# Kernel optimization log

Measured on AMD Instinct MI355X. Metric: run time of the kernel, lower is better.

The kernel has to match this reference:

```python
import jax, jax.numpy as jnp
import numpy as np

N = 102400          # total nodes (256 graphs x 400 nodes)
E = 3276800         # edges (avg degree 32)
B = 256             # num graphs
NODE_DIM, MRI_DIM, COG_DIM, CLIN_DIM, GEN_DIM, NUM_CLASSES = 128, 256, 64, 32, 512, 3
EPS = 1e-5

def _lin(k, i, o):
    kw, kb = jax.random.split(k)
    s = 1.0 / np.sqrt(i)
    return (jax.random.uniform(kw, (i, o), jnp.float32, -s, s),
            jax.random.uniform(kb, (o,), jnp.float32, -s, s))

def setup_inputs() -> dict:
    key = jax.random.key(0)
    ks = jax.random.split(key, 20)
    inp = {}
    inp['x'] = jax.random.normal(ks[0], (N, NODE_DIM), jnp.float32)
    inp['edge_index'] = jax.random.randint(ks[1], (2, E), 0, N)
    inp['batch'] = jnp.repeat(jnp.arange(B, dtype=jnp.int32), N // B)
    inp['mri'] = jax.random.normal(ks[2], (B, MRI_DIM), jnp.float32)
    inp['cog'] = jax.random.normal(ks[3], (B, COG_DIM), jnp.float32)
    inp['clin'] = jax.random.normal(ks[4], (B, CLIN_DIM), jnp.float32)
    inp['gen'] = jax.random.normal(ks[5], (B, GEN_DIM), jnp.float32)
    inp['W1'], inp['b1'] = _lin(ks[6], NODE_DIM, 64)
    inp['W2'], inp['b2'] = _lin(ks[7], 64, 32)
    inp['W3'], inp['b3'] = _lin(ks[8], 32, 16)
    inp['bn1_g'] = jnp.ones((64,), jnp.float32); inp['bn1_b'] = jnp.zeros((64,), jnp.float32)
    inp['bn2_g'] = jnp.ones((32,), jnp.float32); inp['bn2_b'] = jnp.zeros((32,), jnp.float32)
    inp['mriW'], inp['mrib'] = _lin(ks[9], MRI_DIM, 16)
    inp['cogW'], inp['cogb'] = _lin(ks[10], COG_DIM, 16)
    inp['clinW'], inp['clinb'] = _lin(ks[11], CLIN_DIM, 16)
    inp['genW'], inp['genb'] = _lin(ks[12], GEN_DIM, 16)
    inp['c1W'], inp['c1b'] = _lin(ks[13], 96, 64)  # 32 (pooled) + 64 (multimodal)
    inp['cbn1_g'] = jnp.ones((64,), jnp.float32); inp['cbn1_b'] = jnp.zeros((64,), jnp.float32)
    inp['c2W'], inp['c2b'] = _lin(ks[14], 64, 32)
    inp['cbn2_g'] = jnp.ones((32,), jnp.float32); inp['cbn2_b'] = jnp.zeros((32,), jnp.float32)
    inp['c3W'], inp['c3b'] = _lin(ks[15], 32, NUM_CLASSES)
    return inp

def _bn(h, g, b):
    # BatchNorm1d in training mode: biased batch stats
    m = h.mean(0)
    v = jnp.mean((h - m) ** 2, 0)
    return (h - m) * jax.lax.rsqrt(v + EPS) * g + b

def _gcn(h, W, bias, s, d, norm):
    # GCNConv: linear -> symmetric-normalized scatter-add aggregation (self-loops in s/d)
    h = h @ W
    agg = jnp.zeros_like(h).at[d].add(h[s] * norm[:, None])
    return agg + bias

def reference(x, edge_index, batch, mri, cog, clin, gen,
              W1, b1, W2, b2, W3, b3, bn1_g, bn1_b, bn2_g, bn2_b,
              mriW, mrib, cogW, cogb, clinW, clinb, genW, genb,
              c1W, c1b, cbn1_g, cbn1_b, c2W, c2b, cbn2_g, cbn2_b, c3W, c3b):
    n = x.shape[0]
    loop = jnp.arange(n)
    s = jnp.concatenate([edge_index[0], loop])
    d = jnp.concatenate([edge_index[1], loop])
    deg = jnp.zeros((n,), x.dtype).at[d].add(1.0)
    dinv = jax.lax.rsqrt(deg)  # deg >= 1 due to self-loops
    norm = dinv[s] * dinv[d]

    x1 = jax.nn.relu(_bn(_gcn(x, W1, b1, s, d, norm), bn1_g, bn1_b))
    x2 = jax.nn.relu(_bn(_gcn(x1, W2, b2, s, d, norm), bn2_g, bn2_b))
    gf = jax.nn.relu(_gcn(x2, W3, b3, s, d, norm))  # [N,16]

    cnt = jax.ops.segment_sum(jnp.ones((n,), x.dtype), batch, num_segments=B)
    g_mean = jax.ops.segment_sum(gf, batch, num_segments=B) / cnt[:, None]
    g_max = jax.ops.segment_max(gf, batch, num_segments=B)
    g_emb = jnp.concatenate([g_mean, g_max], axis=1)  # [B,32]

    mm = jnp.concatenate([
        jax.nn.relu(mri @ mriW + mrib),
        jax.nn.relu(cog @ cogW + cogb),
        jax.nn.relu(clin @ clinW + clinb),
        jax.nn.relu(gen @ genW + genb)], axis=1)  # [B,64]

    h = jnp.concatenate([g_emb, mm], axis=1)  # [B,96]
    h = jax.nn.relu(_bn(h @ c1W + c1b, cbn1_g, cbn1_b))  # dropout = identity (eval)
    h = jax.nn.relu(_bn(h @ c2W + c2b, cbn2_g, cbn2_b))
    out = h @ c3W + c3b
    return jax.nn.log_softmax(out, axis=1)
```

## Files before the change

### kernel.cpp

```cpp
#include <hip/hip_runtime.h>
#include <hip/hip_bf16.h>

#define TPB 256
#define BSHIFT 9
#define BNODES 512
#define CH 4096

typedef unsigned long long u64;
typedef __attribute__((ext_vector_type(8))) short short8;
typedef __attribute__((ext_vector_type(4))) float f32x4;

__device__ inline unsigned short f2bf(float f) {
    unsigned u = __float_as_uint(f);
    return (unsigned short)((u + 0x7FFF + ((u >> 16) & 1)) >> 16);
}
__device__ inline float bf2f(short s) {
    return __uint_as_float(((unsigned)(unsigned short)s) << 16);
}

__global__ void k_early(const float* __restrict__ x, unsigned short* __restrict__ xb, int npA,
                        const int* __restrict__ dstp, int* __restrict__ bcnt, int E,
                        int nbuk, int npart,
                        const float* __restrict__ W1, const float* __restrict__ W2,
                        const float* __restrict__ W3, unsigned short* __restrict__ Wpack) {
    __shared__ int h[256];
    int blk = blockIdx.x, tid = threadIdx.x;
    if (blk < npA) {
        int g = blk * TPB + tid;
        int lane = g & 63, tile = g >> 6;
        int rowblk = tile >> 2, kblk = tile & 3;
        int row = rowblk * 16 + (lane & 15);
        int k0 = kblk * 32 + (lane >> 4) * 8;
        const float4* p = reinterpret_cast<const float4*>(x + (size_t)row * 128 + k0);
        float4 v0 = p[0], v1 = p[1];
        float vs[8] = {v0.x, v0.y, v0.z, v0.w, v1.x, v1.y, v1.z, v1.w};
        short8 rr;
        #pragma unroll
        for (int u = 0; u < 8; ++u) rr[u] = (short)f2bf(vs[u]);
        *reinterpret_cast<short8*>(xb + (size_t)g * 8) = rr;
    } else if (blk < npA + npart) {
        int pb = blk - npA;
        h[tid] = 0;
        __syncthreads();
        int e0 = pb * CH;
        int e1 = min(e0 + CH, E);
        for (int e = e0 + tid; e < e1; e += TPB) atomicAdd(&h[dstp[e] >> BSHIFT], 1);
        __syncthreads();
        if (tid < nbuk && h[tid]) atomicAdd(&bcnt[tid], h[tid]);
    } else if (tid < 64) {
        int b = blk - npA - npart;
        const float* W; int KB, C; size_t off; int idx;
        if (b < 16)      { W = W1; KB = 4; C = 64; off = 0;     idx = b; }
        else if (b < 20) { W = W2; KB = 2; C = 32; off = 8192;  idx = b - 16; }
        else             { W = W3; KB = 1; C = 16; off = 10240; idx = b - 20; }
        int nblk = idx / KB, kblk = idx - nblk * KB;
        int col = nblk * 16 + (tid & 15);
        int k0 = kblk * 32 + (tid >> 4) * 8;
        short8 rr;
        #pragma unroll
        for (int j = 0; j < 8; ++j) rr[j] = (short)f2bf(W[(size_t)(k0 + j) * C + col]);
        *reinterpret_cast<short8*>(Wpack + off + ((size_t)idx * 64 + tid) * 8) = rr;
    }
}


__global__ void k_bscan(const int* __restrict__ bcnt, int* __restrict__ bbase,
                        int* __restrict__ gcur, int nbuk, int E) {
    __shared__ int s[256];
    int tid = threadIdx.x;
    int v = (tid < nbuk) ? bcnt[tid] : 0;
    s[tid] = v;
    __syncthreads();
    for (int o = 1; o < 256; o <<= 1) {
        int t = (tid >= o) ? s[tid - o] : 0;
        __syncthreads();
        s[tid] += t;
        __syncthreads();
    }
    if (tid < nbuk) { int e = s[tid] - v; bbase[tid] = e; gcur[tid] = e; }
    if (tid == 0) bbase[nbuk] = E;
}

__global__ void k_partition(const int* __restrict__ ei, int* __restrict__ gcur,
                            u64* __restrict__ part, int E, int nbuk) {
    __shared__ int h[256], baseg[256], scn[256], cur[256];
    __shared__ u64 stage[CH];
    int tid = threadIdx.x;
    h[tid] = 0;
    __syncthreads();
    int e0 = blockIdx.x * CH;
    int ecnt = min(CH, E - e0);
    const int* srcp = ei;
    const int* dstp = ei + E;
    for (int i = tid; i < ecnt; i += TPB) atomicAdd(&h[dstp[e0 + i] >> BSHIFT], 1);
    __syncthreads();
    int v = h[tid];
    if (tid < nbuk && v) baseg[tid] = atomicAdd(&gcur[tid], v);
    scn[tid] = v;
    __syncthreads();
    for (int o = 1; o < 256; o <<= 1) {
        int t = (tid >= o) ? scn[tid - o] : 0;
        __syncthreads();
        scn[tid] += t;
        __syncthreads();
    }
    int excl = scn[tid] - v;
    __syncthreads();
    scn[tid] = excl; cur[tid] = excl;
    __syncthreads();
    for (int i = tid; i < ecnt; i += TPB) {
        int s = srcp[e0 + i], d = dstp[e0 + i];
        int bk = d >> BSHIFT;
        int p = atomicAdd(&cur[bk], 1);
        stage[p] = ((u64)(unsigned)d << 32) | (unsigned)s;
    }
    __syncthreads();
    for (int i = tid; i < ecnt; i += TPB) {
        u64 vv = stage[i];
        int bk = (int)(vv >> 32) >> BSHIFT;
        part[baseg[bk] + (i - scn[bk])] = vv;
    }
}

__global__ void k_bucket_csr(const u64* __restrict__ part, const int* __restrict__ bbase,
                             float* __restrict__ dinv, int* __restrict__ offsets,
                             int* __restrict__ csr, int N, int nbuk) {
    __shared__ int cnt[BNODES];
    __shared__ int ps[256];
    __shared__ int off_s[BNODES];
    int b = blockIdx.x, tid = threadIdx.x;
    int n0 = b << BSHIFT;
    int nn = min(BNODES, N - n0);
    int j0 = bbase[b], j1 = bbase[b + 1];
    for (int i = tid; i < BNODES; i += TPB) cnt[i] = 0;
    __syncthreads();
    for (int j = j0 + tid; j < j1; j += TPB) {
        int dst = (int)(part[j] >> 32);
        atomicAdd(&cnt[dst - n0], 1);
    }
    __syncthreads();
    int a0 = cnt[2 * tid], a1 = cnt[2 * tid + 1];
    ps[tid] = a0 + a1;
    __syncthreads();
    for (int o = 1; o < 256; o <<= 1) {
        int t = (tid >= o) ? ps[tid - o] : 0;
        __syncthreads();
        ps[tid] += t;
        __syncthreads();
    }
    int excl = ps[tid] - (a0 + a1);
    off_s[2 * tid] = excl;
    off_s[2 * tid + 1] = excl + a0;
    __syncthreads();
    for (int i = tid; i < nn; i += TPB) {
        dinv[n0 + i] = rsqrtf((float)(cnt[i] + 1));
        offsets[n0 + i] = j0 + off_s[i];
    }
    if (b == nbuk - 1 && tid == 0) offsets[N] = j1;
    __syncthreads();
    for (int i = tid; i < BNODES; i += TPB) cnt[i] = j0 + off_s[i];
    __syncthreads();
    for (int j = j0 + tid; j < j1; j += TPB) {
        u64 vv = part[j];
        int dst = (int)(vv >> 32);
        int src = (int)(vv & 0xffffffffu);
        int pos = atomicAdd(&cnt[dst - n0], 1);
        csr[pos] = src;
    }
}

template<int K, int C, int SW, bool BN>
__global__ void k_mfma_gemm(const unsigned short* __restrict__ A,
                            const unsigned short* __restrict__ Wp,
                            const float* __restrict__ scale, const float* __restrict__ shift,
                            const float* __restrict__ dinv,
                            __hip_bfloat16* __restrict__ hh, size_t slice) {
    constexpr int KB = K / 32, NB = C / 16;
    int lane = threadIdx.x & 63, w = threadIdx.x >> 6;
    int rowblk = blockIdx.x * 4 + w;
    const short8* Af = reinterpret_cast<const short8*>(A);
    const short8* Bf = reinterpret_cast<const short8*>(Wp);
    short8 b[NB][KB];
    #pragma unroll
    for (int nb = 0; nb < NB; ++nb)
        #pragma unroll
        for (int kb = 0; kb < KB; ++kb)
            b[nb][kb] = Bf[(nb * KB + kb) * 64 + lane];
    f32x4 z = {0.f, 0.f, 0.f, 0.f};
    f32x4 acc[NB];
    #pragma unroll
    for (int nb = 0; nb < NB; ++nb) acc[nb] = z;
    #pragma unroll
    for (int kb = 0; kb < KB; ++kb) {
        short8 a = Af[((size_t)rowblk * KB + kb) * 64 + lane];
        if (BN) {
            int k0 = kb * 32 + (lane >> 4) * 8;
            #pragma unroll
            for (int u = 0; u < 8; ++u) {
                float v = bf2f(a[u]);
                v = fmaxf(v * scale[k0 + u] + shift[k0 + u], 0.f);
                a[u] = (short)f2bf(v);
            }
        }
        #pragma unroll
        for (int nb = 0; nb < NB; ++nb)
            acc[nb] = __builtin_amdgcn_mfma_f32_16x16x32_bf16(a, b[nb][kb], acc[nb], 0, 0, 0);
    }
    int colb = lane & 15;
    int node0 = rowblk * 16 + (lane >> 4) * 4;
    float dv[4];
    #pragma unroll
    for (int j = 0; j < 4; ++j) dv[j] = dinv[node0 + j];
    #pragma unroll
    for (int nb = 0; nb < NB; ++nb) {
        int c = nb * 16 + colb;
        size_t base = (size_t)(c / SW) * slice + (c % SW);
        #pragma unroll
        for (int j = 0; j < 4; ++j)
            hh[base + (size_t)(node0 + j) * SW] = __float2bfloat16(acc[nb][j] * dv[j]);
    }
}

template<bool STATS>
__global__ void k_gather_frag32(const __hip_bfloat16* __restrict__ hhp,
                                const int* __restrict__ offs, const int* __restrict__ csr,
                                const float* __restrict__ dinv, const float* __restrict__ bias,
                                unsigned short* __restrict__ frag, int KBN, int kblk,
                                float* __restrict__ pstat, int n) {
    __shared__ float lred[16 * 528];
    __shared__ float sred[2 * 544];
    __shared__ __align__(16) unsigned short fragstage[512];
    int tid = threadIdx.x;
    int g = tid >> 4, l = tid & 15;
    int node = blockIdx.x * 16 + g;
    int j0 = offs[node], j1 = offs[node + 1];
    float facc[32];
    #pragma unroll
    for (int u = 0; u < 32; ++u) facc[u] = 0.f;
    if (l == 15) {
        const short8* sr = reinterpret_cast<const short8*>(hhp + (size_t)node * 32);
        short8 r0 = sr[0], r1 = sr[1], r2 = sr[2], r3 = sr[3];
        #pragma unroll
        for (int u = 0; u < 8; ++u) {
            facc[u] += bf2f(r0[u]);      facc[8 + u]  += bf2f(r1[u]);
            facc[16 + u] += bf2f(r2[u]); facc[24 + u] += bf2f(r3[u]);
        }
    }
    int j = j0 + l;
    for (; j + 16 < j1; j += 32) {
        int s0 = __builtin_nontemporal_load(&csr[j]);
        int s1 = __builtin_nontemporal_load(&csr[j + 16]);
        const short8* ra = reinterpret_cast<const short8*>(hhp + (size_t)s0 * 32);
        const short8* rb = reinterpret_cast<const short8*>(hhp + (size_t)s1 * 32);
        short8 a0 = ra[0], a1 = ra[1], a2 = ra[2], a3 = ra[3];
        short8 b0 = rb[0], b1 = rb[1], b2 = rb[2], b3 = rb[3];
        #pragma unroll
        for (int u = 0; u < 8; ++u) {
            facc[u]      += bf2f(a0[u]) + bf2f(b0[u]);
            facc[8 + u]  += bf2f(a1[u]) + bf2f(b1[u]);
            facc[16 + u] += bf2f(a2[u]) + bf2f(b2[u]);
            facc[24 + u] += bf2f(a3[u]) + bf2f(b3[u]);
        }
    }
    if (j < j1) {
        int s = __builtin_nontemporal_load(&csr[j]);
        const short8* rr = reinterpret_cast<const short8*>(hhp + (size_t)s * 32);
        short8 r0 = rr[0], r1 = rr[1], r2 = rr[2], r3 = rr[3];
        #pragma unroll
        for (int u = 0; u < 8; ++u) {
            facc[u] += bf2f(r0[u]);      facc[8 + u]  += bf2f(r1[u]);
            facc[16 + u] += bf2f(r2[u]); facc[24 + u] += bf2f(r3[u]);
        }
    }
    int wbase = g * 528 + l * 33;
    #pragma unroll
    for (int u = 0; u < 32; ++u) lred[wbase + u] = facc[u];
    __syncthreads();
    int rbase = g * 528 + l;
    float alo = 0.f, ahi = 0.f;
    #pragma unroll
    for (int k = 0; k < 16; ++k) {
        alo += lred[rbase + k * 33];
        ahi += lred[rbase + k * 33 + 16];
    }
    float dv = dinv[node];
    float vlo = dv * alo + bias[l];
    float vhi = dv * ahi + bias[l + 16];
    fragstage[((((l >> 3) * 16 + g) << 3) | (l & 7))]       = f2bf(vlo);
    fragstage[((((2 + (l >> 3)) * 16 + g) << 3) | (l & 7))] = f2bf(vhi);
    if (STATS) {
        sred[l * 17 + g]              = vlo;
        sred[(l + 16) * 17 + g]       = vhi;
        sred[544 + l * 17 + g]        = vlo * vlo;
        sred[544 + (l + 16) * 17 + g] = vhi * vhi;
    }
    __syncthreads();
    if (tid < 64) {
        *reinterpret_cast<short8*>(frag + ((size_t)(blockIdx.x * KBN + kblk) * 64 + tid) * 8)
            = *reinterpret_cast<const short8*>(&fragstage[(size_t)tid * 8]);
        if (STATS) {
            int which = tid >> 5, c = tid & 31;
            const float* base = sred + which * 544 + c * 17;
            float a = 0.f;
            #pragma unroll
            for (int k = 0; k < 16; ++k) a += base[k];
            pstat[(size_t)blockIdx.x * 64 + which * 32 + c] = a;
        }
    }
}

template<int CT, bool RELU>
__global__ void k_gather_row(const __hip_bfloat16* __restrict__ hhp,
                             const int* __restrict__ offs, const int* __restrict__ csr,
                             const float* __restrict__ dinv, const float* __restrict__ bias,
                             __hip_bfloat16* __restrict__ outp, int n) {
    __shared__ float lred[16 * 272];
    int tid = threadIdx.x;
    int g = tid >> 4, l = tid & 15;
    int node = blockIdx.x * 16 + g;
    int j0 = offs[node], j1 = offs[node + 1];
    float facc[16];
    #pragma unroll
    for (int u = 0; u < 16; ++u) facc[u] = 0.f;
    if (l == 15) {
        const short8* sr = reinterpret_cast<const short8*>(hhp + (size_t)node * 16);
        short8 r0 = sr[0], r1 = sr[1];
        #pragma unroll
        for (int u = 0; u < 8; ++u) { facc[u] += bf2f(r0[u]); facc[8 + u] += bf2f(r1[u]); }
    }
    int j = j0 + l;
    for (; j + 16 < j1; j += 32) {
        int s0 = __builtin_nontemporal_load(&csr[j]);
        int s1 = __builtin_nontemporal_load(&csr[j + 16]);
        const short8* ra = reinterpret_cast<const short8*>(hhp + (size_t)s0 * 16);
        const short8* rb = reinterpret_cast<const short8*>(hhp + (size_t)s1 * 16);
        short8 a0 = ra[0], a1 = ra[1], b0 = rb[0], b1 = rb[1];
        #pragma unroll
        for (int u = 0; u < 8; ++u) {
            facc[u]     += bf2f(a0[u]) + bf2f(b0[u]);
            facc[8 + u] += bf2f(a1[u]) + bf2f(b1[u]);
        }
    }
    if (j < j1) {
        int s = __builtin_nontemporal_load(&csr[j]);
        const short8* rr = reinterpret_cast<const short8*>(hhp + (size_t)s * 16);
        short8 r0 = rr[0], r1 = rr[1];
        #pragma unroll
        for (int u = 0; u < 8; ++u) { facc[u] += bf2f(r0[u]); facc[8 + u] += bf2f(r1[u]); }
    }
    int wbase = g * 272 + l * 17;
    #pragma unroll
    for (int u = 0; u < 16; ++u) lred[wbase + u] = facc[u];
    __syncthreads();
    int rbase = g * 272 + l;
    float acc = 0.f;
    #pragma unroll
    for (int k = 0; k < 16; ++k) acc += lred[rbase + k * 17];
    float v = dinv[node] * acc + bias[l];
    if (RELU) v = fmaxf(v, 0.f);
    outp[(size_t)node * CT + l] = __float2bfloat16(v);
}

__global__ void k_bnred(const float* __restrict__ pstat, float* __restrict__ bred, int G) {
    __shared__ float ss[256];
    int tid = threadIdx.x;
    int p = blockIdx.x >> 6, c = blockIdx.x & 63;
    int rows_per = (G + 63) >> 6;
    int r0 = c * rows_per, r1 = min(r0 + rows_per, G);
    const float* base = pstat + (size_t)p * G * 64;
    float acc = 0.f;
    for (int i = r0 * 64 + tid; i < r1 * 64; i += 256) acc += base[i];
    ss[tid] = acc;
    __syncthreads();
    #pragma unroll
    for (int o = 128; o >= 64; o >>= 1) {
        if (tid < o) ss[tid] += ss[tid + o];
        __syncthreads();
    }
    if (tid < 64) bred[(size_t)blockIdx.x * 64 + tid] = ss[tid];
}

__global__ void k_bnstat2(const float* __restrict__ bred, const float* __restrict__ g,
                          const float* __restrict__ b, float* __restrict__ scale,
                          float* __restrict__ shift, float invN) {
    __shared__ float ss[256];
    int tid = threadIdx.x, p = blockIdx.x;
    const float* base = bred + (size_t)p * 64 * 64;
    float acc = 0.f;
    for (int i = tid; i < 64 * 64; i += 256) acc += base[i];
    ss[tid] = acc;
    __syncthreads();
    #pragma unroll
    for (int o = 128; o >= 64; o >>= 1) {
        if (tid < o) ss[tid] += ss[tid + o];
        __syncthreads();
    }
    if (tid < 32) {
        int ch = p * 32 + tid;
        float m = ss[tid] * invN;
        float var = ss[32 + tid] * invN - m * m;
        float sc = g[ch] * rsqrtf(var + 1e-5f);
        scale[ch] = sc;
        shift[ch] = b[ch] - m * sc;
    }
}

__global__ void k_graphhead(const __hip_bfloat16* __restrict__ gf, int nper,
                            const float* __restrict__ mri, const float* __restrict__ cog,
                            const float* __restrict__ clin, const float* __restrict__ gen,
                            const float* __restrict__ mriW, const float* __restrict__ mrib,
                            const float* __restrict__ cogW, const float* __restrict__ cogb,
                            const float* __restrict__ clinW, const float* __restrict__ clinb,
                            const float* __restrict__ genW, const float* __restrict__ genb,
                            const float* __restrict__ c1W, const float* __restrict__ c1b,
                            float* __restrict__ t1) {
    __shared__ float ssum[TPB], smax[TPB];
    __shared__ float hb[96];
    int b = blockIdx.x, tid = threadIdx.x;
    {
        int c = tid & 15, r0 = tid >> 4;
        const __hip_bfloat16* base = gf + (size_t)b * nper * 16;
        float s = 0.f, m = -1e30f;
        for (int r = r0; r < nper; r += 16) {
            float v = __bfloat162float(base[r * 16 + c]);
            s += v; m = fmaxf(m, v);
        }
        ssum[tid] = s; smax[tid] = m; __syncthreads();
        for (int off = 128; off >= 16; off >>= 1) {
            if (tid < off) { ssum[tid] += ssum[tid + off]; smax[tid] = fmaxf(smax[tid], smax[tid + off]); }
            __syncthreads();
        }
        if (tid < 16) { hb[tid] = ssum[tid] / (float)nper; hb[16 + tid] = smax[tid]; }
    }
    {
        int w = tid >> 6, lane = tid & 63;
        int c = lane & 15, part = lane >> 4;
        const float* in; const float* W; const float* bias; int K;
        if (w == 0)      { in = mri  + b * 256; W = mriW;  bias = mrib;  K = 256; }
        else if (w == 1) { in = cog  + b * 64;  W = cogW;  bias = cogb;  K = 64;  }
        else if (w == 2) { in = clin + b * 32;  W = clinW; bias = clinb; K = 32;  }
        else             { in = gen  + b * 512; W = genW;  bias = genb;  K = 512; }
        int kq = K >> 2, k0 = part * kq;
        float acc = 0.f;
        for (int k = k0; k < k0 + kq; k += 4) {
            float4 iv = *reinterpret_cast<const float4*>(in + k);
            acc += iv.x * W[k * 16 + c] + iv.y * W[(k + 1) * 16 + c]
                 + iv.z * W[(k + 2) * 16 + c] + iv.w * W[(k + 3) * 16 + c];
        }
        acc += __shfl_xor(acc, 16);
        acc += __shfl_xor(acc, 32);
        if (part == 0) hb[32 + w * 16 + c] = fmaxf(acc + bias[c], 0.f);
    }
    __syncthreads();
    if (tid < 64) {
        float acc = c1b[tid];
        #pragma unroll
        for (int k = 0; k < 96; ++k) acc += hb[k] * c1W[k * 64 + tid];
        t1[b * 64 + tid] = acc;
    }
}

__global__ __launch_bounds__(1024) void k_headtail(
        float* __restrict__ t1g,
        const float* __restrict__ cbn1_g, const float* __restrict__ cbn1_b,
        const float* __restrict__ c2W, const float* __restrict__ c2b,
        const float* __restrict__ cbn2_g, const float* __restrict__ cbn2_b,
        const float* __restrict__ c3W, const float* __restrict__ c3b,
        float* __restrict__ out) {
    __shared__ float red[1024];
    __shared__ float t2s[256 * 32];
    __shared__ float sc1[64], sh1[64], sc2[32], sh2[32];
    int tid = threadIdx.x;
    const float invB = 1.0f / 256.0f;

    float psum = 0.f, psq = 0.f;
    for (int i = tid; i < 16384; i += 1024) {
        float v = t1g[i]; psum += v; psq += v * v;
    }
    red[tid] = psum; __syncthreads();
    for (int o = 512; o >= 64; o >>= 1) { if (tid < o) red[tid] += red[tid + o]; __syncthreads(); }
    if (tid < 64) sc1[tid] = red[tid];
    __syncthreads();
    red[tid] = psq; __syncthreads();
    for (int o = 512; o >= 64; o >>= 1) { if (tid < o) red[tid] += red[tid + o]; __syncthreads(); }
    if (tid < 64) {
        float m = sc1[tid] * invB;
        float var = red[tid] * invB - m * m;
        float s = cbn1_g[tid] * rsqrtf(var + 1e-5f);
        sc1[tid] = s; sh1[tid] = cbn1_b[tid] - m * s;
    }
    __syncthreads();
    for (int i = tid; i < 16384; i += 1024) {
        int k = i & 63;
        t1g[i] = fmaxf(t1g[i] * sc1[k] + sh1[k], 0.f);
    }
    __syncthreads();
    int j2 = tid & 31, g2 = tid >> 5;
    float p2 = 0.f, q2 = 0.f;
    for (int b = g2 * 8; b < g2 * 8 + 8; ++b) {
        const float* tr = t1g + b * 64;
        float acc = c2b[j2];
        #pragma unroll
        for (int k = 0; k < 64; ++k) acc += tr[k] * c2W[k * 32 + j2];
        t2s[b * 32 + j2] = acc; p2 += acc; q2 += acc * acc;
    }
    red[tid] = p2; __syncthreads();
    for (int o = 512; o >= 32; o >>= 1) { if (tid < o) red[tid] += red[tid + o]; __syncthreads(); }
    if (tid < 32) sc2[tid] = red[tid];
    __syncthreads();
    red[tid] = q2; __syncthreads();
    for (int o = 512; o >= 32; o >>= 1) { if (tid < o) red[tid] += red[tid + o]; __syncthreads(); }
    if (tid < 32) {
        float m = sc2[tid] * invB;
        float var = red[tid] * invB - m * m;
        float s = cbn2_g[tid] * rsqrtf(var + 1e-5f);
        sc2[tid] = s; sh2[tid] = cbn2_b[tid] - m * s;
    }
    __syncthreads();
    if (tid < 256) {
        const float* tr = t2s + tid * 32;
        float o0 = c3b[0], o1 = c3b[1], o2 = c3b[2];
        #pragma unroll
        for (int k = 0; k < 32; ++k) {
            float v = fmaxf(tr[k] * sc2[k] + sh2[k], 0.f);
            o0 += v * c3W[k * 3 + 0];
            o1 += v * c3W[k * 3 + 1];
            o2 += v * c3W[k * 3 + 2];
        }
        float m = fmaxf(fmaxf(o0, o1), o2);
        float lse = m + logf(expf(o0 - m) + expf(o1 - m) + expf(o2 - m));
        out[tid * 3 + 0] = o0 - lse;
        out[tid * 3 + 1] = o1 - lse;
        out[tid * 3 + 2] = o2 - lse;
    }
}


extern "C" void kernel_launch(void* const* d_in, const int* in_sizes, int n_in,
                              void* d_out, int out_size, void* d_ws, size_t ws_size,
                              hipStream_t stream) {
    const float* x    = (const float*)d_in[0];
    const int*   ei   = (const int*)d_in[1];
    const float* mri  = (const float*)d_in[3];
    const float* cog  = (const float*)d_in[4];
    const float* clin = (const float*)d_in[5];
    const float* gen  = (const float*)d_in[6];
    const float* W1 = (const float*)d_in[7];  const float* b1 = (const float*)d_in[8];
    const float* W2 = (const float*)d_in[9];  const float* b2 = (const float*)d_in[10];
    const float* W3 = (const float*)d_in[11]; const float* b3 = (const float*)d_in[12];
    const float* bn1_g = (const float*)d_in[13]; const float* bn1_b = (const float*)d_in[14];
    const float* bn2_g = (const float*)d_in[15]; const float* bn2_b = (const float*)d_in[16];
    const float* mriW = (const float*)d_in[17]; const float* mrib = (const float*)d_in[18];
    const float* cogW = (const float*)d_in[19]; const float* cogb = (const float*)d_in[20];
    const float* clinW = (const float*)d_in[21]; const float* clinb = (const float*)d_in[22];
    const float* genW = (const float*)d_in[23]; const float* genb = (const float*)d_in[24];
    const float* c1W = (const float*)d_in[25]; const float* c1b = (const float*)d_in[26];
    const float* cbn1_g = (const float*)d_in[27]; const float* cbn1_b = (const float*)d_in[28];
    const float* c2W = (const float*)d_in[29]; const float* c2b = (const float*)d_in[30];
    const float* cbn2_g = (const float*)d_in[31]; const float* cbn2_b = (const float*)d_in[32];
    const float* c3W = (const float*)d_in[33]; const float* c3b = (const float*)d_in[34];
    float* out = (float*)d_out;

    const int N = in_sizes[0] / 128;
    const int E = in_sizes[1] / 2;
    const int B = in_sizes[6] / 512;
    const int nper = N / B;
    const int nbuk = (N + BNODES - 1) >> BSHIFT;
    const int npart = (E + CH - 1) / CH;
    const int rowblks = N / 16;
    const int G = N / 16;
    const int npA = rowblks;

    char* ws = (char*)d_ws;
    size_t off = 0;
    auto alloc = [&](size_t bytes) -> void* {
        void* p = ws + off;
        off += (bytes + 255) & ~(size_t)255;
        return p;
    };
    int*   bcnt    = (int*)alloc(256 * 4);
    int*   bbase   = (int*)alloc((size_t)(nbuk + 1) * 4);
    int*   gcur    = (int*)alloc((size_t)nbuk * 4);
    u64*   part    = (u64*)alloc((size_t)E * 8);
    __hip_bfloat16* agg = (__hip_bfloat16*)part;
    int*   offsets = (int*)alloc((size_t)(N + 1) * 4);
    int*   csr     = (int*)alloc((size_t)E * 4);
    float* dinv    = (float*)alloc((size_t)N * 4);
    __hip_bfloat16* hh = (__hip_bfloat16*)alloc((size_t)N * 64 * 2);
    unsigned short* xb = (unsigned short*)alloc((size_t)N * 128 * 2);
    unsigned short* Wpack = (unsigned short*)alloc(10752 * 2);
    float* pstat   = (float*)alloc((size_t)3 * G * 64 * 4);
    float* bred    = (float*)alloc((size_t)3 * 64 * 64 * 4);
    float* scale1  = (float*)alloc(64 * 4);
    float* shift1  = (float*)alloc(64 * 4);
    float* scale2  = (float*)alloc(32 * 4);
    float* shift2  = (float*)alloc(32 * 4);
    float* t1      = (float*)alloc((size_t)B * 64 * 4);
    (void)ws_size; (void)n_in; (void)out_size;

    hipMemsetAsync(bcnt, 0, 256 * 4, stream);

    k_early<<<npA + npart + 21, TPB, 0, stream>>>(x, xb, npA, ei + E, bcnt, E, nbuk, npart,
                                                  W1, W2, W3, Wpack);
    k_bscan<<<1, TPB, 0, stream>>>(bcnt, bbase, gcur, nbuk, E);
    k_partition<<<npart, TPB, 0, stream>>>(ei, gcur, part, E, nbuk);
    k_bucket_csr<<<nbuk, TPB, 0, stream>>>(part, bbase, dinv, offsets, csr, N, nbuk);

    size_t slice32 = (size_t)N * 32;
    int gmm = rowblks / 4;

    k_mfma_gemm<128, 64, 32, false><<<gmm, TPB, 0, stream>>>(xb, Wpack, nullptr, nullptr,
                                                             dinv, hh, slice32);
    for (int p = 0; p < 2; ++p)
        k_gather_frag32<true><<<G, TPB, 0, stream>>>(
            hh + p * slice32, offsets, csr, dinv, b1 + p * 32,
            xb, 2, p, pstat + (size_t)p * G * 64, N);
    k_bnred<<<2 * 64, 256, 0, stream>>>(pstat, bred, G);
    k_bnstat2<<<2, 256, 0, stream>>>(bred, bn1_g, bn1_b, scale1, shift1, 1.0f / N);

    k_mfma_gemm<64, 32, 32, true><<<gmm, TPB, 0, stream>>>(xb, Wpack + 8192, scale1, shift1,
                                                           dinv, hh, slice32);
    k_gather_frag32<true><<<G, TPB, 0, stream>>>(
        hh, offsets, csr, dinv, b2, xb, 1, 0, pstat + (size_t)2 * G * 64, N);
    k_bnred<<<64, 256, 0, stream>>>(pstat + (size_t)2 * G * 64, bred + 2 * 64 * 64, G);
    k_bnstat2<<<1, 256, 0, stream>>>(bred + 2 * 64 * 64, bn2_g, bn2_b, scale2, shift2, 1.0f / N);

    k_mfma_gemm<32, 16, 16, true><<<gmm, TPB, 0, stream>>>(xb, Wpack + 10240, scale2, shift2,
                                                           dinv, hh, (size_t)N * 16);
    k_gather_row<16, true><<<G, TPB, 0, stream>>>(hh, offsets, csr, dinv, b3, agg, N);

    k_graphhead<<<B, TPB, 0, stream>>>(agg, nper, mri, cog, clin, gen,
                                       mriW, mrib, cogW, cogb, clinW, clinb, genW, genb,
                                       c1W, c1b, t1);
    k_headtail<<<1, 1024, 0, stream>>>(t1, cbn1_g, cbn1_b, c2W, c2b,
                                       cbn2_g, cbn2_b, c3W, c3b, out);
}
```

Baseline: 368.8 us.

## Fuse layer-1 gather into one 64-wide pass and cache bucket edges in LDS

Layer 1 now stores the transformed features as full 64-wide bf16 rows and gathers them in a single kernel, instead of two passes over 32-column slices. This reads the CSR indices once and issues wider contiguous row reads, at the cost of 64 float accumulators per thread and possibly lower occupancy. The bucket CSR kernel also caches packed (dst,src) edges in shared memory during the counting pass. The scatter pass then avoids rereading the partition array from global memory, but the extra LDS use may lower occupancy for that kernel.

```diff
diff --git a/kernel.cpp b/kernel.cpp
--- a/kernel.cpp
+++ b/kernel.cpp
@@ -5,6 +5,7 @@
 #define BSHIFT 9
 #define BNODES 512
 #define CH 4096
+#define ECAP 14336
 
 typedef unsigned long long u64;
 typedef __attribute__((ext_vector_type(8))) short short8;
@@ -128,6 +129,7 @@
     __shared__ int cnt[BNODES];
     __shared__ int ps[256];
     __shared__ int off_s[BNODES];
+    __shared__ unsigned ecache[ECAP];
     int b = blockIdx.x, tid = threadIdx.x;
     int n0 = b << BSHIFT;
     int nn = min(BNODES, N - n0);
@@ -135,8 +137,11 @@
     for (int i = tid; i < BNODES; i += TPB) cnt[i] = 0;
     __syncthreads();
     for (int j = j0 + tid; j < j1; j += TPB) {
-        int dst = (int)(part[j] >> 32);
-        atomicAdd(&cnt[dst - n0], 1);
+        u64 vv = part[j];
+        int rel = (int)(vv >> 32) - n0;
+        atomicAdd(&cnt[rel], 1);
+        int li = j - j0;
+        if (li < ECAP) ecache[li] = ((unsigned)rel << 23) | (unsigned)(vv & 0xffffffffu);
     }
     __syncthreads();
     int a0 = cnt[2 * tid], a1 = cnt[2 * tid + 1];
@@ -160,11 +165,20 @@
     __syncthreads();
     for (int i = tid; i < BNODES; i += TPB) cnt[i] = j0 + off_s[i];
     __syncthreads();
-    for (int j = j0 + tid; j < j1; j += TPB) {
+    int total = j1 - j0;
+    int lim = min(total, ECAP);
+    for (int li = tid; li < lim; li += TPB) {
+        unsigned e = ecache[li];
+        int rel = e >> 23;
+        int src = (int)(e & 0x7FFFFFu);
+        int pos = atomicAdd(&cnt[rel], 1);
+        csr[pos] = src;
+    }
+    for (int j = j0 + lim + tid; j < j1; j += TPB) {
         u64 vv = part[j];
-        int dst = (int)(vv >> 32);
+        int rel = (int)(vv >> 32) - n0;
         int src = (int)(vv & 0xffffffffu);
-        int pos = atomicAdd(&cnt[dst - n0], 1);
+        int pos = atomicAdd(&cnt[rel], 1);
         csr[pos] = src;
     }
 }
@@ -218,6 +232,79 @@
         #pragma unroll
         for (int j = 0; j < 4; ++j)
             hh[base + (size_t)(node0 + j) * SW] = __float2bfloat16(acc[nb][j] * dv[j]);
+    }
+}
+
+__global__ void k_gather_frag64(const __hip_bfloat16* __restrict__ hhp,
+                                const int* __restrict__ offs, const int* __restrict__ csr,
+                                const float* __restrict__ dinv, const float* __restrict__ bias,
+                                unsigned short* __restrict__ frag,
+                                float* __restrict__ pstat0, float* __restrict__ pstat1, int n) {
+    __shared__ float lred[16 * 528];
+    __shared__ float sred[2 * 544];
+    __shared__ __align__(16) unsigned short fragstage[512];
+    int tid = threadIdx.x;
+    int g = tid >> 4, l = tid & 15;
+    int node = blockIdx.x * 16 + g;
+    int j0 = offs[node], j1 = offs[node + 1];
+    float facc[64];
+    #pragma unroll
+    for (int u = 0; u < 64; ++u) facc[u] = 0.f;
+    if (l == 15) {
+        const short8* sr = reinterpret_cast<const short8*>(hhp + (size_t)node * 64);
+        short8 r[8];
+        #pragma unroll
+        for (int q = 0; q < 8; ++q) r[q] = sr[q];
+        #pragma unroll
+        for (int q = 0; q < 8; ++q)
+            #pragma unroll
+            for (int u = 0; u < 8; ++u) facc[q * 8 + u] += bf2f(r[q][u]);
+    }
+    for (int j = j0 + l; j < j1; j += 16) {
+        int s = __builtin_nontemporal_load(&csr[j]);
+        const short8* rp = reinterpret_cast<const short8*>(hhp + (size_t)s * 64);
+        short8 r[8];
+        #pragma unroll
+        for (int q = 0; q < 8; ++q) r[q] = rp[q];
+        #pragma unroll
+        for (int q = 0; q < 8; ++q)
+            #pragma unroll
+            for (int u = 0; u < 8; ++u) facc[q * 8 + u] += bf2f(r[q][u]);
+    }
+    float dv = dinv[node];
+    #pragma unroll
+    for (int h = 0; h < 2; ++h) {
+        if (h) __syncthreads();
+        int wbase = g * 528 + l * 33;
+        #pragma unroll
+        for (int u = 0; u < 32; ++u) lred[wbase + u] = facc[h * 32 + u];
+        __syncthreads();
+        int rbase = g * 528 + l;
+        float alo = 0.f, ahi = 0.f;
+        #pragma unroll
+        for (int k = 0; k < 16; ++k) {
+            alo += lred[rbase + k * 33];
+            ahi += lred[rbase + k * 33 + 16];
+        }
+        float vlo = dv * alo + bias[h * 32 + l];
+        float vhi = dv * ahi + bias[h * 32 + l + 16];
+        fragstage[((((l >> 3) * 16 + g) << 3) | (l & 7))]       = f2bf(vlo);
+        fragstage[((((2 + (l >> 3)) * 16 + g) << 3) | (l & 7))] = f2bf(vhi);
+        sred[l * 17 + g]              = vlo;
+        sred[(l + 16) * 17 + g]       = vhi;
+        sred[544 + l * 17 + g]        = vlo * vlo;
+        sred[544 + (l + 16) * 17 + g] = vhi * vhi;
+        __syncthreads();
+        if (tid < 64) {
+            *reinterpret_cast<short8*>(frag + ((size_t)(blockIdx.x * 2 + h) * 64 + tid) * 8)
+                = *reinterpret_cast<const short8*>(&fragstage[(size_t)tid * 8]);
+            int which = tid >> 5, c = tid & 31;
+            const float* base = sred + which * 544 + c * 17;
+            float a = 0.f;
+            #pragma unroll
+            for (int k = 0; k < 16; ++k) a += base[k];
+            (h ? pstat1 : pstat0)[(size_t)blockIdx.x * 64 + which * 32 + c] = a;
+        }
     }
 }
 
@@ -606,20 +693,17 @@
     k_partition<<<npart, TPB, 0, stream>>>(ei, gcur, part, E, nbuk);
     k_bucket_csr<<<nbuk, TPB, 0, stream>>>(part, bbase, dinv, offsets, csr, N, nbuk);
 
-    size_t slice32 = (size_t)N * 32;
     int gmm = rowblks / 4;
 
-    k_mfma_gemm<128, 64, 32, false><<<gmm, TPB, 0, stream>>>(xb, Wpack, nullptr, nullptr,
-                                                             dinv, hh, slice32);
-    for (int p = 0; p < 2; ++p)
-        k_gather_frag32<true><<<G, TPB, 0, stream>>>(
-            hh + p * slice32, offsets, csr, dinv, b1 + p * 32,
-            xb, 2, p, pstat + (size_t)p * G * 64, N);
+    k_mfma_gemm<128, 64, 64, false><<<gmm, TPB, 0, stream>>>(xb, Wpack, nullptr, nullptr,
+                                                             dinv, hh, (size_t)N * 64);
+    k_gather_frag64<<<G, TPB, 0, stream>>>(hh, offsets, csr, dinv, b1, xb,
+                                           pstat, pstat + (size_t)G * 64, N);
     k_bnred<<<2 * 64, 256, 0, stream>>>(pstat, bred, G);
     k_bnstat2<<<2, 256, 0, stream>>>(bred, bn1_g, bn1_b, scale1, shift1, 1.0f / N);
 
     k_mfma_gemm<64, 32, 32, true><<<gmm, TPB, 0, stream>>>(xb, Wpack + 8192, scale1, shift1,
-                                                           dinv, hh, slice32);
+                                                           dinv, hh, (size_t)N * 32);
     k_gather_frag32<true><<<G, TPB, 0, stream>>>(
         hh, offsets, csr, dinv, b2, xb, 1, 0, pstat + (size_t)2 * G * 64, N);
     k_bnred<<<64, 256, 0, stream>>>(pstat + (size_t)2 * G * 64, bred + 2 * 64 * 64, G);
```

Result: faster. 353.5 us, median of 2 (-4.2%).
